# Kernel optimization log

Measured on AMD Instinct MI355X. Metric: run time of the kernel, lower is better.

Reference implementation:

```python
import jax, jax.numpy as jnp
import numpy as np

D_MODEL = 2048
N_HEADS = 16
HEAD_DIM = D_MODEL // N_HEADS
D_FF = ((int(8 * D_MODEL / 3) + 64) // 64) * 64  # 5504
B, T = 2, 2048
EPS = 1e-8
NEG = -1e9


def rotate_half(x):
    half = x.shape[-1] // 2
    return jnp.concatenate([-x[..., half:], x[..., :half]], axis=-1)


def apply_rope(x, cos, sin):
    # x: [B,H,T,hd]; cos/sin: [T,hd] -> [1,1,T,hd]
    c = cos[None, None, :, :]
    s = sin[None, None, :, :]
    return x * c + rotate_half(x) * s


def rmsnorm(x, w):
    rms = jnp.sqrt(jnp.mean(x * x, axis=-1, keepdims=True))
    return w * x / (rms + EPS)


def setup_inputs() -> dict:
    key = jax.random.key(0)
    ks = jax.random.split(key, 12)
    x = jax.random.normal(ks[0], (B, T, D_MODEL), dtype=jnp.float32)
    # RoPE tables
    inv_freq = 1.0 / (10000.0 ** (jnp.arange(0, HEAD_DIM, 2, dtype=jnp.float32) / HEAD_DIM))
    pos = jnp.arange(T, dtype=jnp.float32)
    freqs = pos[:, None] * inv_freq[None, :]          # [T, hd/2]
    emb = jnp.concatenate([freqs, freqs], axis=-1)    # [T, hd]
    cos, sin = jnp.cos(emb), jnp.sin(emb)
    # causal additive mask [T,T]
    mask = jnp.where(jnp.tril(jnp.ones((T, T), dtype=bool)), 0.0, NEG).astype(jnp.float32)
    scale = 0.02
    Wq = jax.random.normal(ks[1], (D_MODEL, D_MODEL), dtype=jnp.float32) * scale
    Wk = jax.random.normal(ks[2], (D_MODEL, D_MODEL), dtype=jnp.float32) * scale
    Wv = jax.random.normal(ks[3], (D_MODEL, D_MODEL), dtype=jnp.float32) * scale
    Wo = jax.random.normal(ks[4], (D_MODEL, D_MODEL), dtype=jnp.float32) * scale
    W1 = jax.random.normal(ks[5], (D_FF, D_MODEL), dtype=jnp.float32) * scale
    W2 = jax.random.normal(ks[6], (D_FF, D_MODEL), dtype=jnp.float32) * scale
    Wout = jax.random.normal(ks[7], (D_MODEL, D_FF), dtype=jnp.float32) * scale
    g1 = jnp.ones((D_MODEL,), dtype=jnp.float32)
    g2 = jnp.ones((D_MODEL,), dtype=jnp.float32)
    return {"x": x, "cos": cos, "sin": sin, "mask": mask,
            "g1": g1, "g2": g2, "Wq": Wq, "Wk": Wk, "Wv": Wv, "Wo": Wo,
            "W1": W1, "W2": W2, "Wout": Wout}


def reference(x, cos, sin, mask, g1, g2, Wq, Wk, Wv, Wo, W1, W2, Wout):
    Bb, Tt, Dd = x.shape

    def split_heads(t):  # [B,T,D] -> [B,H,T,hd]
        return t.reshape(Bb, Tt, N_HEADS, HEAD_DIM).transpose(0, 2, 1, 3)

    h = rmsnorm(x, g1)
    Q = apply_rope(split_heads(h @ Wq.T), cos, sin)
    K = apply_rope(split_heads(h @ Wk.T), cos, sin)
    V = split_heads(h @ Wv.T)
    scores = jnp.einsum('bhqd,bhkd->bhqk', Q, K) / jnp.sqrt(jnp.float32(HEAD_DIM))
    scores = scores + mask  # broadcast [T,T] over [B,H,T,T]
    weights = jax.nn.softmax(scores, axis=-1)
    attn = jnp.einsum('bhqk,bhkd->bhqd', weights, V)
    attn = attn.transpose(0, 2, 1, 3).reshape(Bb, Tt, Dd)
    x = x + attn @ Wo.T

    h2 = rmsnorm(x, g2)
    ff = (jax.nn.silu(h2 @ W1.T) * (h2 @ W2.T)) @ Wout.T
    return x + ff
```

## Files before the change

kernel.cpp:

```cpp
#include <hip/hip_runtime.h>


using bf16 = __bf16;
typedef __bf16 bf16x2 __attribute__((ext_vector_type(2)));
typedef __bf16 bf16x8 __attribute__((ext_vector_type(8)));
typedef float f32x4 __attribute__((ext_vector_type(4)));

#define MFMA_BF16(a, b, c) __builtin_amdgcn_mfma_f32_16x16x32_bf16((a), (b), (c), 0, 0, 0)

__device__ __forceinline__ void gld_lds16(const void* g, void* l) {
  __builtin_amdgcn_global_load_lds((const __attribute__((address_space(1))) void*)g,
                                   (__attribute__((address_space(3))) void*)l,
                                   16, 0, 0);
}

__global__ void detect_dtype(const unsigned int* __restrict__ X, int* __restrict__ flag) {
  const int tid = threadIdx.x;
  const unsigned int w = X[tid];
  const unsigned int e_lo = (w >> 7) & 0xFF;
  const unsigned int e_hi = (w >> 23) & 0xFF;
  const bool sane = (e_lo >= 97u && e_lo <= 157u) && (e_hi >= 97u && e_hi <= 157u);
  const unsigned long long m = __ballot(sane);
  if (tid == 0) *flag = (__popcll(m) > 48) ? 1 : 0;
}

__global__ __launch_bounds__(256) void convert_in(const void* __restrict__ src,
                                                  bf16* __restrict__ dst,
                                                  const int* __restrict__ flag) {
  const size_t i = ((size_t)blockIdx.x * 256 + threadIdx.x) * 8;
  if (*flag) {
    *(bf16x8*)(dst + i) = *(const bf16x8*)((const bf16*)src + i);
  } else {
    const float* s = (const float*)src;
    float4 a = *(const float4*)(s + i);
    float4 b = *(const float4*)(s + i + 4);
    bf16x8 o;
    o[0] = (bf16)a.x; o[1] = (bf16)a.y; o[2] = (bf16)a.z; o[3] = (bf16)a.w;
    o[4] = (bf16)b.x; o[5] = (bf16)b.y; o[6] = (bf16)b.z; o[7] = (bf16)b.w;
    *(bf16x8*)(dst + i) = o;
  }
}

__global__ __launch_bounds__(256) void rmsnorm_bf16(const bf16* __restrict__ X,
                                                    const bf16* __restrict__ g,
                                                    bf16* __restrict__ Hout) {
  const int row = blockIdx.x, tid = threadIdx.x;
  const size_t off = (size_t)row * 2048 + tid * 8;
  bf16x8 x8 = *(const bf16x8*)(X + off);
  float v[8];
  float s = 0.f;
#pragma unroll
  for (int j = 0; j < 8; ++j) { v[j] = (float)x8[j]; s += v[j] * v[j]; }
#pragma unroll
  for (int o = 32; o; o >>= 1) s += __shfl_xor(s, o);
  __shared__ float red[4];
  if ((tid & 63) == 0) red[tid >> 6] = s;
  __syncthreads();
  const float tot = red[0] + red[1] + red[2] + red[3];
  const float inv = 1.f / (sqrtf(tot * (1.f / 2048.f)) + 1e-8f);
  bf16x8 g8 = *(const bf16x8*)(g + tid * 8);
  bf16x8 o8;
#pragma unroll
  for (int j = 0; j < 8; ++j) o8[j] = (bf16)((float)g8[j] * v[j] * inv);
  *(bf16x8*)(Hout + off) = o8;
}

__global__ __launch_bounds__(256) void rmsnorm_f32(const float* __restrict__ X,
                                                   const bf16* __restrict__ g,
                                                   bf16* __restrict__ Hout) {
  const int row = blockIdx.x, tid = threadIdx.x;
  const size_t off = (size_t)row * 2048 + tid * 8;
  float4 a0 = *(const float4*)(X + off);
  float4 a1 = *(const float4*)(X + off + 4);
  float v[8] = {a0.x, a0.y, a0.z, a0.w, a1.x, a1.y, a1.z, a1.w};
  float s = 0.f;
#pragma unroll
  for (int j = 0; j < 8; ++j) s += v[j] * v[j];
#pragma unroll
  for (int o = 32; o; o >>= 1) s += __shfl_xor(s, o);
  __shared__ float red[4];
  if ((tid & 63) == 0) red[tid >> 6] = s;
  __syncthreads();
  const float tot = red[0] + red[1] + red[2] + red[3];
  const float inv = 1.f / (sqrtf(tot * (1.f / 2048.f)) + 1e-8f);
  bf16x8 g8 = *(const bf16x8*)(g + tid * 8);
  bf16x8 o8;
#pragma unroll
  for (int j = 0; j < 8; ++j) o8[j] = (bf16)((float)g8[j] * v[j] * inv);
  *(bf16x8*)(Hout + off) = o8;
}

__global__ __launch_bounds__(256) void rope_k(bf16* __restrict__ Q, bf16* __restrict__ Kg,
                                              const bf16* __restrict__ cosb,
                                              const bf16* __restrict__ sinb) {
  const int tid = threadIdx.x;
  const int rr = tid >> 7;
  const int c = tid & 127;
  const int bt = blockIdx.x * 2 + rr;
  const int t = bt & 2047;
  const int h = c >> 3;
  const int d0 = (c & 7) * 8;
  const size_t row = (size_t)bt * 2048;
  const int i0 = h * 128 + d0;
  bf16x8 c0 = *(const bf16x8*)(cosb + t * 128 + d0);
  bf16x8 c1 = *(const bf16x8*)(cosb + t * 128 + d0 + 64);
  bf16x8 s0 = *(const bf16x8*)(sinb + t * 128 + d0);
  bf16x8 s1 = *(const bf16x8*)(sinb + t * 128 + d0 + 64);
  bf16x8 qa = *(const bf16x8*)(Q + row + i0);
  bf16x8 qb = *(const bf16x8*)(Q + row + i0 + 64);
  bf16x8 ka = *(const bf16x8*)(Kg + row + i0);
  bf16x8 kb = *(const bf16x8*)(Kg + row + i0 + 64);
  bf16x8 qo0, qo1, ko0, ko1;
#pragma unroll
  for (int j = 0; j < 8; ++j) {
    float cj0 = (float)c0[j], cj1 = (float)c1[j];
    float sj0 = (float)s0[j], sj1 = (float)s1[j];
    float qaj = (float)qa[j], qbj = (float)qb[j];
    float kaj = (float)ka[j], kbj = (float)kb[j];
    qo0[j] = (bf16)(qaj * cj0 - qbj * sj0);
    qo1[j] = (bf16)(qbj * cj1 + qaj * sj1);
    ko0[j] = (bf16)(kaj * cj0 - kbj * sj0);
    ko1[j] = (bf16)(kbj * cj1 + kaj * sj1);
  }
  *(bf16x8*)(Q + row + i0) = qo0;
  *(bf16x8*)(Q + row + i0 + 64) = qo1;
  *(bf16x8*)(Kg + row + i0) = ko0;
  *(bf16x8*)(Kg + row + i0 + 64) = ko1;
}

template <int EPI>
__global__ __launch_bounds__(256) void gemm_bt(const bf16* __restrict__ A,
                                               const bf16* __restrict__ W,
                                               bf16* __restrict__ Cb, float* __restrict__ Cf,
                                               const bf16* __restrict__ resb,
                                               const float* __restrict__ resf,
                                               const bf16* __restrict__ mulb,
                                               const int* __restrict__ oflag,
                                               int M, int N, int K) {
  __shared__ bf16 As[3][128 * 32];
  __shared__ bf16 Ws[3][128 * 32];
  const int tid = threadIdx.x;
  const int wave = tid >> 6, lane = tid & 63;
  const int quad = lane >> 4, l15 = lane & 15;
  const int wm = wave >> 1, wn = wave & 1;
  const int m0 = blockIdx.y * 128, n0 = blockIdx.x * 128;

  f32x4 acc[4][4];
#pragma unroll
  for (int i = 0; i < 4; ++i)
#pragma unroll
    for (int j = 0; j < 4; ++j) acc[i][j] = {0.f, 0.f, 0.f, 0.f};

  const bf16* Ab = A + (size_t)m0 * K;
  const bf16* Wb = W + (size_t)n0 * K;
  const int sr = lane & 15;
  const int sc = (lane >> 4) * 8;

  auto stage = [&](int buf, int kb) {
    const int k0 = kb << 5;
#pragma unroll
    for (int c = 0; c < 2; ++c) {
      const int g = wave * 2 + c;
      gld_lds16(Ab + (size_t)(g * 16 + sr) * K + k0 + sc, (char*)As[buf] + g * 1024);
      gld_lds16(Wb + (size_t)(g * 16 + sr) * K + k0 + sc, (char*)Ws[buf] + g * 1024);
    }
  };
  auto compute = [&](int buf) {
    bf16x8 af[4], wf[4];
#pragma unroll
    for (int mt = 0; mt < 4; ++mt)
      af[mt] = *(const bf16x8*)((const char*)As[buf] + (wm * 4 + mt) * 1024 + lane * 16);
#pragma unroll
    for (int nt = 0; nt < 4; ++nt)
      wf[nt] = *(const bf16x8*)((const char*)Ws[buf] + (wn * 4 + nt) * 1024 + lane * 16);
    __builtin_amdgcn_s_setprio(1);
#pragma unroll
    for (int mt = 0; mt < 4; ++mt)
#pragma unroll
      for (int nt = 0; nt < 4; ++nt)
        acc[mt][nt] = MFMA_BF16(af[mt], wf[nt], acc[mt][nt]);
    __builtin_amdgcn_s_setprio(0);
  };

  const int nk = K >> 5;
  stage(0, 0);
  stage(1, 1);
  int bc = 0, bn2 = 2;
  for (int kb = 0; kb < nk - 1; ++kb) {
    asm volatile("s_waitcnt vmcnt(4)" ::: "memory");
    __builtin_amdgcn_s_barrier();
    __builtin_amdgcn_sched_barrier(0);
    if (kb + 2 < nk) stage(bn2, kb + 2);
    compute(bc);
    bc = (bc == 2) ? 0 : bc + 1;
    bn2 = (bn2 == 2) ? 0 : bn2 + 1;
  }
  asm volatile("s_waitcnt vmcnt(0)" ::: "memory");
  __builtin_amdgcn_s_barrier();
  __builtin_amdgcn_sched_barrier(0);
  compute(bc);

  const int obf = (EPI == 4 && oflag) ? *oflag : 0;
#pragma unroll
  for (int mt = 0; mt < 4; ++mt) {
#pragma unroll
    for (int nt = 0; nt < 4; ++nt) {
#pragma unroll
      for (int r = 0; r < 4; ++r) {
        const int row = m0 + wm * 64 + mt * 16 + quad * 4 + r;
        const int col = n0 + wn * 64 + nt * 16 + l15;
        const size_t idx = (size_t)row * N + col;
        const float v = acc[mt][nt][r];
        if constexpr (EPI == 0) {
          Cb[idx] = (bf16)v;
        } else if constexpr (EPI == 1) {
          Cf[idx] = v + (float)resb[idx];
        } else if constexpr (EPI == 2) {
          Cb[idx] = (bf16)(v / (1.f + __expf(-v)));
        } else if constexpr (EPI == 3) {
          Cb[idx] = (bf16)((float)mulb[idx] * v);
        } else {
          const float rres = resf[idx] + v;
          if (obf) Cb[idx] = (bf16)rres;
          else     Cf[idx] = rres;
        }
      }
    }
  }
}

__global__ __launch_bounds__(256) void flash_attn(const bf16* __restrict__ Q,
                                                  const bf16* __restrict__ Kg,
                                                  const bf16* __restrict__ Vg,
                                                  bf16* __restrict__ O) {
  __shared__ bf16 Ks[2][64 * 128];
  __shared__ bf16 Vt[128 * 64];
  __shared__ bf16 Ps[4 * 16 * 64];
  const int tid = threadIdx.x;
  const int wave = tid >> 6, lane = tid & 63;
  const int quad = lane >> 4, l15 = lane & 15;
  const int bh = blockIdx.x;
  const int b = bh >> 4, h = bh & 15;
  const size_t base = (size_t)b * 2048 * 2048 + h * 128;
  const float scale = 0.08838834764831845f;

  bf16x8 vva[2], vvb[2];

  auto stageK = [&](int buf, int kb) {
    const int k0 = kb * 64;
#pragma unroll
    for (int c = 0; c < 4; ++c) {
      const int ch = tid + 256 * c;
      const int row = ch >> 4;
      const int scb = ((ch & 15) * 16) ^ ((row & 7) << 4);
      gld_lds16((const char*)(Kg + base + (size_t)(k0 + row) * 2048) + scb,
                (char*)Ks[buf] + wave * 1024 + c * 4096);
    }
  };
  auto loadV = [&](int kb) {
    const int k0 = kb * 64;
#pragma unroll
    for (int c = 0; c < 2; ++c) {
      const int tau = tid + 256 * c;
      const int kp = tau & 31;
      const int d0 = (tau >> 5) * 8;
      vva[c] = *(const bf16x8*)(Vg + base + (size_t)(k0 + 2 * kp) * 2048 + d0);
      vvb[c] = *(const bf16x8*)(Vg + base + (size_t)(k0 + 2 * kp + 1) * 2048 + d0);
    }
  };
  auto writeV = [&]() {
#pragma unroll
    for (int c = 0; c < 2; ++c) {
      const int tau = tid + 256 * c;
      const int kp = tau & 31;
      const int d0 = (tau >> 5) * 8;
#pragma unroll
      for (int j = 0; j < 8; ++j) {
        bf16x2 pr = {vva[c][j], vvb[c][j]};
        const int d = d0 + j;
        *(bf16x2*)((char*)Vt + d * 128 + ((4 * kp) ^ ((d & 7) << 4))) = pr;
      }
    }
  };

#pragma unroll 1
  for (int half = 0; half < 2; ++half) {
    const int qt = half ? (31 - (int)blockIdx.y) : (int)blockIdx.y;
    const int q0 = qt * 64;

    bf16x8 qf[4];
    {
      const bf16* qrow = Q + base + (size_t)(q0 + wave * 16 + l15) * 2048;
#pragma unroll
      for (int ks = 0; ks < 4; ++ks) qf[ks] = *(const bf16x8*)(qrow + ks * 32 + quad * 8);
    }

    f32x4 o[8];
#pragma unroll
    for (int i = 0; i < 8; ++i) o[i] = {0.f, 0.f, 0.f, 0.f};
    float m_r[4] = {-1e30f, -1e30f, -1e30f, -1e30f};
    float l_r[4] = {0.f, 0.f, 0.f, 0.f};

    loadV(0);
    stageK(0, 0);
    if (qt >= 1) stageK(1, 1);
    asm volatile("s_waitcnt vmcnt(4)" ::: "memory");
    __builtin_amdgcn_s_barrier();
    __builtin_amdgcn_sched_barrier(0);

#pragma unroll 1
    for (int kb = 0; kb <= qt; ++kb) {
      const int cur = kb & 1;
      const int k0 = kb * 64;

      writeV();
      if (kb + 1 <= qt) loadV(kb + 1);

      f32x4 s[4];
      __builtin_amdgcn_s_setprio(1);
#pragma unroll
      for (int nt = 0; nt < 4; ++nt) {
        s[nt] = {0.f, 0.f, 0.f, 0.f};
        const int krow = nt * 16 + l15;
#pragma unroll
        for (int ks = 0; ks < 4; ++ks) {
          bf16x8 kf = *(const bf16x8*)((char*)Ks[cur] + krow * 256 +
                                       ((ks * 64 + quad * 16) ^ ((krow & 7) << 4)));
          s[nt] = MFMA_BF16(qf[ks], kf, s[nt]);
        }
      }
      __builtin_amdgcn_s_setprio(0);

      float sv[4][4];
#pragma unroll
      for (int nt = 0; nt < 4; ++nt) {
#pragma unroll
        for (int r = 0; r < 4; ++r) {
          float v = s[nt][r] * scale;
          const int key = k0 + nt * 16 + l15;
          const int qq = q0 + wave * 16 + quad * 4 + r;
          if (key > qq) v = -1e9f;
          sv[nt][r] = v;
        }
      }

#pragma unroll
      for (int r = 0; r < 4; ++r) {
        float rmax = fmaxf(fmaxf(sv[0][r], sv[1][r]), fmaxf(sv[2][r], sv[3][r]));
#pragma unroll
        for (int off = 1; off < 16; off <<= 1) rmax = fmaxf(rmax, __shfl_xor(rmax, off));
        const float mnew = fmaxf(m_r[r], rmax);
        const float alpha = __expf(m_r[r] - mnew);
        float psum = 0.f;
        const int qrow = quad * 4 + r;
#pragma unroll
        for (int nt = 0; nt < 4; ++nt) {
          const float p = __expf(sv[nt][r] - mnew);
          psum += p;
          *(bf16*)((char*)Ps + wave * 2048 + qrow * 128 +
                   ((2 * (nt * 16 + l15)) ^ ((qrow & 7) << 4))) = (bf16)p;
        }
#pragma unroll
        for (int off = 1; off < 16; off <<= 1) psum += __shfl_xor(psum, off);
        l_r[r] = l_r[r] * alpha + psum;
        m_r[r] = mnew;
#pragma unroll
        for (int nt2 = 0; nt2 < 8; ++nt2) o[nt2][r] *= alpha;
      }

      asm volatile("s_waitcnt lgkmcnt(0)" ::: "memory");
      __builtin_amdgcn_s_barrier();
      __builtin_amdgcn_sched_barrier(0);

      if (kb + 2 <= qt) stageK(cur, kb + 2);

      __builtin_amdgcn_s_setprio(1);
#pragma unroll
      for (int ks2 = 0; ks2 < 2; ++ks2) {
        bf16x8 pf = *(const bf16x8*)((char*)Ps + wave * 2048 + l15 * 128 +
                                     ((ks2 * 64 + quad * 16) ^ ((l15 & 7) << 4)));
#pragma unroll
        for (int nt2 = 0; nt2 < 8; ++nt2) {
          const int drow = nt2 * 16 + l15;
          bf16x8 vf = *(const bf16x8*)((char*)Vt + drow * 128 +
                                       ((ks2 * 64 + quad * 16) ^ ((drow & 7) << 4)));
          o[nt2] = MFMA_BF16(pf, vf, o[nt2]);
        }
      }
      __builtin_amdgcn_s_setprio(0);

      asm volatile("s_waitcnt lgkmcnt(0)" ::: "memory");
      asm volatile("s_waitcnt vmcnt(8)" ::: "memory");
      __builtin_amdgcn_s_barrier();
      __builtin_amdgcn_sched_barrier(0);
    }

#pragma unroll
    for (int nt2 = 0; nt2 < 8; ++nt2) {
#pragma unroll
      for (int r = 0; r < 4; ++r) {
        const int qq = q0 + wave * 16 + quad * 4 + r;
        const int dd = nt2 * 16 + l15;
        O[base + (size_t)qq * 2048 + dd] = (bf16)(o[nt2][r] / l_r[r]);
      }
    }
  }
}

extern "C" void kernel_launch(void* const* d_in, const int* in_sizes, int n_in,
                              void* d_out, int out_size, void* d_ws, size_t ws_size,
                              hipStream_t stream) {
  const void* x_raw = d_in[0];
  const void* cos_raw = d_in[1];
  const void* sin_raw = d_in[2];
  const void* g1_raw = d_in[4];
  const void* g2_raw = d_in[5];
  const void* W_raw[7] = {d_in[6], d_in[7], d_in[8], d_in[9], d_in[10], d_in[11], d_in[12]};

  char* ws = (char*)d_ws;
  const size_t MB = 1048576ull;
  int* flag = (int*)ws;
  bf16* g1c = (bf16*)(ws + 4096);
  bf16* g2c = (bf16*)(ws + 12288);
  bf16* cosc = (bf16*)(ws + 65536);
  bf16* sinc = (bf16*)(ws + 655360);
  bf16* xc   = (bf16*)(ws + 2 * MB);
  bf16* wslot= (bf16*)(ws + 18 * MB);
  bf16* hbuf = (bf16*)(ws + 41 * MB);
  bf16* qbuf = (bf16*)(ws + 57 * MB);
  bf16* kbuf = (bf16*)(ws + 73 * MB);
  bf16* vbuf = (bf16*)(ws + 89 * MB);
  bf16* abuf = (bf16*)(ws + 105 * MB);
  float* x1  = (float*)(ws + 57 * MB);
  bf16* h2   = (bf16*)(ws + 41 * MB);
  bf16* ubuf = (bf16*)(ws + 89 * MB);

  const int M = 4096;
  dim3 blk(256);

  detect_dtype<<<1, 64, 0, stream>>>((const unsigned int*)x_raw, flag);

  convert_in<<<4096, blk, 0, stream>>>(x_raw, xc, flag);
  convert_in<<<128, blk, 0, stream>>>(cos_raw, cosc, flag);
  convert_in<<<128, blk, 0, stream>>>(sin_raw, sinc, flag);
  convert_in<<<1, blk, 0, stream>>>(g1_raw, g1c, flag);
  convert_in<<<1, blk, 0, stream>>>(g2_raw, g2c, flag);

  rmsnorm_bf16<<<M, blk, 0, stream>>>(xc, g1c, hbuf);

  convert_in<<<2048, blk, 0, stream>>>(W_raw[0], wslot, flag);
  gemm_bt<0><<<dim3(16, 32), blk, 0, stream>>>(hbuf, wslot, qbuf, nullptr, nullptr, nullptr, nullptr, nullptr, M, 2048, 2048);
  convert_in<<<2048, blk, 0, stream>>>(W_raw[1], wslot, flag);
  gemm_bt<0><<<dim3(16, 32), blk, 0, stream>>>(hbuf, wslot, kbuf, nullptr, nullptr, nullptr, nullptr, nullptr, M, 2048, 2048);
  convert_in<<<2048, blk, 0, stream>>>(W_raw[2], wslot, flag);
  gemm_bt<0><<<dim3(16, 32), blk, 0, stream>>>(hbuf, wslot, vbuf, nullptr, nullptr, nullptr, nullptr, nullptr, M, 2048, 2048);

  rope_k<<<M / 2, blk, 0, stream>>>(qbuf, kbuf, cosc, sinc);
  flash_attn<<<dim3(32, 16), blk, 0, stream>>>(qbuf, kbuf, vbuf, abuf);

  convert_in<<<2048, blk, 0, stream>>>(W_raw[3], wslot, flag);
  gemm_bt<1><<<dim3(16, 32), blk, 0, stream>>>(abuf, wslot, nullptr, x1, xc, nullptr, nullptr, nullptr, M, 2048, 2048);

  rmsnorm_f32<<<M, blk, 0, stream>>>(x1, g2c, h2);

  convert_in<<<5504, blk, 0, stream>>>(W_raw[4], wslot, flag);
  gemm_bt<2><<<dim3(43, 32), blk, 0, stream>>>(h2, wslot, ubuf, nullptr, nullptr, nullptr, nullptr, nullptr, M, 5504, 2048);
  convert_in<<<5504, blk, 0, stream>>>(W_raw[5], wslot, flag);
  gemm_bt<3><<<dim3(43, 32), blk, 0, stream>>>(h2, wslot, ubuf, nullptr, nullptr, nullptr, ubuf, nullptr, M, 5504, 2048);
  convert_in<<<5504, blk, 0, stream>>>(W_raw[6], wslot, flag);
  gemm_bt<4><<<dim3(16, 32), blk, 0, stream>>>(ubuf, wslot, (bf16*)d_out, (float*)d_out, nullptr, x1, nullptr, flag, M, 2048, 5504);
}
```

Before: 1.215 ms.

## Enlarge GEMM tiles to 256x128 with 512 threads and BK=64

The GEMM kernel now uses 8 waves per block computing a 256x128 output tile, with the K step doubled to 64 and a triple-buffered LDS pipeline sized for it. Launch grids are halved in M to match. The aim is more operand reuse per loaded tile and fewer barriers per unit of K. In exchange, LDS use per block grows to about 144 KB, which limits occupancy, and there are fewer blocks in flight. The N=5504 launches also still rely on a grid of 43 column tiles, so edge handling stays as before.

```diff
diff --git a/kernel.cpp b/kernel.cpp
--- a/kernel.cpp
+++ b/kernel.cpp
@@ -129,7 +129,7 @@
 }
 
 template <int EPI>
-__global__ __launch_bounds__(256) void gemm_bt(const bf16* __restrict__ A,
+__global__ __launch_bounds__(512) void gemm_bt(const bf16* __restrict__ A,
                                                const bf16* __restrict__ W,
                                                bf16* __restrict__ Cb, float* __restrict__ Cf,
                                                const bf16* __restrict__ resb,
@@ -137,13 +137,13 @@
                                                const bf16* __restrict__ mulb,
                                                const int* __restrict__ oflag,
                                                int M, int N, int K) {
-  __shared__ bf16 As[3][128 * 32];
-  __shared__ bf16 Ws[3][128 * 32];
+  __shared__ bf16 As[3][256 * 64];
+  __shared__ bf16 Ws[3][128 * 64];
   const int tid = threadIdx.x;
   const int wave = tid >> 6, lane = tid & 63;
   const int quad = lane >> 4, l15 = lane & 15;
   const int wm = wave >> 1, wn = wave & 1;
-  const int m0 = blockIdx.y * 128, n0 = blockIdx.x * 128;
+  const int m0 = blockIdx.y * 256, n0 = blockIdx.x * 128;
 
   f32x4 acc[4][4];
 #pragma unroll
@@ -156,49 +156,57 @@
   const int sr = lane & 15;
   const int sc = (lane >> 4) * 8;
 
-  auto stage = [&](int buf, int kb) {
-    const int k0 = kb << 5;
+  auto stage = [&](int buf, int t) {
+    const int k0 = t << 6;
+#pragma unroll
+    for (int c = 0; c < 4; ++c) {
+      const int r = wave * 4 + c;
+      const int g = r >> 1, ks = r & 1;
+      gld_lds16(Ab + (size_t)(g * 16 + sr) * K + k0 + ks * 32 + sc,
+                (char*)As[buf] + r * 1024);
+    }
 #pragma unroll
     for (int c = 0; c < 2; ++c) {
-      const int g = wave * 2 + c;
-      gld_lds16(Ab + (size_t)(g * 16 + sr) * K + k0 + sc, (char*)As[buf] + g * 1024);
-      gld_lds16(Wb + (size_t)(g * 16 + sr) * K + k0 + sc, (char*)Ws[buf] + g * 1024);
+      const int r = wave * 2 + c;
+      const int g = r >> 1, ks = r & 1;
+      gld_lds16(Wb + (size_t)(g * 16 + sr) * K + k0 + ks * 32 + sc,
+                (char*)Ws[buf] + r * 1024);
     }
   };
+
   auto compute = [&](int buf) {
-    bf16x8 af[4], wf[4];
-#pragma unroll
-    for (int mt = 0; mt < 4; ++mt)
-      af[mt] = *(const bf16x8*)((const char*)As[buf] + (wm * 4 + mt) * 1024 + lane * 16);
-#pragma unroll
-    for (int nt = 0; nt < 4; ++nt)
-      wf[nt] = *(const bf16x8*)((const char*)Ws[buf] + (wn * 4 + nt) * 1024 + lane * 16);
-    __builtin_amdgcn_s_setprio(1);
-#pragma unroll
-    for (int mt = 0; mt < 4; ++mt)
+#pragma unroll
+    for (int ks = 0; ks < 2; ++ks) {
+      bf16x8 af[4], wf[4];
+#pragma unroll
+      for (int mt = 0; mt < 4; ++mt)
+        af[mt] = *(const bf16x8*)((const char*)As[buf] +
+                                  ((wm * 4 + mt) * 2 + ks) * 1024 + lane * 16);
 #pragma unroll
       for (int nt = 0; nt < 4; ++nt)
-        acc[mt][nt] = MFMA_BF16(af[mt], wf[nt], acc[mt][nt]);
-    __builtin_amdgcn_s_setprio(0);
+        wf[nt] = *(const bf16x8*)((const char*)Ws[buf] +
+                                  ((wn * 4 + nt) * 2 + ks) * 1024 + lane * 16);
+      __builtin_amdgcn_s_setprio(1);
+#pragma unroll
+      for (int mt = 0; mt < 4; ++mt)
+#pragma unroll
+        for (int nt = 0; nt < 4; ++nt)
+          acc[mt][nt] = MFMA_BF16(af[mt], wf[nt], acc[mt][nt]);
+      __builtin_amdgcn_s_setprio(0);
+    }
   };
 
-  const int nk = K >> 5;
+  const int nk = K >> 6;
   stage(0, 0);
   stage(1, 1);
-  int bc = 0, bn2 = 2;
-  for (int kb = 0; kb < nk - 1; ++kb) {
-    asm volatile("s_waitcnt vmcnt(4)" ::: "memory");
+  for (int t = 0; t < nk; ++t) {
+    if (t < nk - 1) asm volatile("s_waitcnt vmcnt(6)" ::: "memory");
+    else            asm volatile("s_waitcnt vmcnt(0)" ::: "memory");
     __builtin_amdgcn_s_barrier();
     __builtin_amdgcn_sched_barrier(0);
-    if (kb + 2 < nk) stage(bn2, kb + 2);
-    compute(bc);
-    bc = (bc == 2) ? 0 : bc + 1;
-    bn2 = (bn2 == 2) ? 0 : bn2 + 1;
+    if (t + 2 < nk) stage((t + 2) % 3, t + 2);
+    compute(t % 3);
   }
-  asm volatile("s_waitcnt vmcnt(0)" ::: "memory");
-  __builtin_amdgcn_s_barrier();
-  __builtin_amdgcn_sched_barrier(0);
-  compute(bc);
 
   const int obf = (EPI == 4 && oflag) ? *oflag : 0;
 #pragma unroll
@@ -437,6 +445,7 @@
 
   const int M = 4096;
   dim3 blk(256);
+  dim3 blk512(512);
 
   detect_dtype<<<1, 64, 0, stream>>>((const unsigned int*)x_raw, flag);
 
@@ -449,24 +458,24 @@
   rmsnorm_bf16<<<M, blk, 0, stream>>>(xc, g1c, hbuf);
 
   convert_in<<<2048, blk, 0, stream>>>(W_raw[0], wslot, flag);
-  gemm_bt<0><<<dim3(16, 32), blk, 0, stream>>>(hbuf, wslot, qbuf, nullptr, nullptr, nullptr, nullptr, nullptr, M, 2048, 2048);
+  gemm_bt<0><<<dim3(16, 16), blk512, 0, stream>>>(hbuf, wslot, qbuf, nullptr, nullptr, nullptr, nullptr, nullptr, M, 2048, 2048);
   convert_in<<<2048, blk, 0, stream>>>(W_raw[1], wslot, flag);
-  gemm_bt<0><<<dim3(16, 32), blk, 0, stream>>>(hbuf, wslot, kbuf, nullptr, nullptr, nullptr, nullptr, nullptr, M, 2048, 2048);
+  gemm_bt<0><<<dim3(16, 16), blk512, 0, stream>>>(hbuf, wslot, kbuf, nullptr, nullptr, nullptr, nullptr, nullptr, M, 2048, 2048);
   convert_in<<<2048, blk, 0, stream>>>(W_raw[2], wslot, flag);
-  gemm_bt<0><<<dim3(16, 32), blk, 0, stream>>>(hbuf, wslot, vbuf, nullptr, nullptr, nullptr, nullptr, nullptr, M, 2048, 2048);
+  gemm_bt<0><<<dim3(16, 16), blk512, 0, stream>>>(hbuf, wslot, vbuf, nullptr, nullptr, nullptr, nullptr, nullptr, M, 2048, 2048);
 
   rope_k<<<M / 2, blk, 0, stream>>>(qbuf, kbuf, cosc, sinc);
   flash_attn<<<dim3(32, 16), blk, 0, stream>>>(qbuf, kbuf, vbuf, abuf);
 
   convert_in<<<2048, blk, 0, stream>>>(W_raw[3], wslot, flag);
-  gemm_bt<1><<<dim3(16, 32), blk, 0, stream>>>(abuf, wslot, nullptr, x1, xc, nullptr, nullptr, nullptr, M, 2048, 2048);
+  gemm_bt<1><<<dim3(16, 16), blk512, 0, stream>>>(abuf, wslot, nullptr, x1, xc, nullptr, nullptr, nullptr, M, 2048, 2048);
 
   rmsnorm_f32<<<M, blk, 0, stream>>>(x1, g2c, h2);
 
   convert_in<<<5504, blk, 0, stream>>>(W_raw[4], wslot, flag);
-  gemm_bt<2><<<dim3(43, 32), blk, 0, stream>>>(h2, wslot, ubuf, nullptr, nullptr, nullptr, nullptr, nullptr, M, 5504, 2048);
+  gemm_bt<2><<<dim3(43, 16), blk512, 0, stream>>>(h2, wslot, ubuf, nullptr, nullptr, nullptr, nullptr, nullptr, M, 5504, 2048);
   convert_in<<<5504, blk, 0, stream>>>(W_raw[5], wslot, flag);
-  gemm_bt<3><<<dim3(43, 32), blk, 0, stream>>>(h2, wslot, ubuf, nullptr, nullptr, nullptr, ubuf, nullptr, M, 5504, 2048);
+  gemm_bt<3><<<dim3(43, 16), blk512, 0, stream>>>(h2, wslot, ubuf, nullptr, nullptr, nullptr, ubuf, nullptr, M, 5504, 2048);
   convert_in<<<5504, blk, 0, stream>>>(W_raw[6], wslot, flag);
-  gemm_bt<4><<<dim3(16, 32), blk, 0, stream>>>(ubuf, wslot, (bf16*)d_out, (float*)d_out, nullptr, x1, nullptr, flag, M, 2048, 5504);
-}
+  gemm_bt<4><<<dim3(16, 16), blk512, 0, stream>>>(ubuf, wslot, (bf16*)d_out, (float*)d_out, nullptr, x1, nullptr, flag, M, 2048, 5504);
+}
```

After: 1.289 ms. +6.1%, slower.
